# Kernel optimization log

Measured on AMD Instinct MI355X. Metric: run time of the kernel, lower is better.

The kernel has to match this reference:

```python
import jax, jax.numpy as jnp
import numpy as np

DIM = 48
NUM_HEADS = 8
DIM_HEAD = DIM // NUM_HEADS
SCALE = DIM_HEAD ** -0.5
EPS = 1e-12  # torch F.normalize eps
DN = ('NCHW', 'OIHW', 'NCHW')


def setup_inputs() -> dict:
    key = jax.random.key(0)
    k1, k2, k3, k4 = jax.random.split(key, 4)
    x = jax.random.normal(k1, (8, DIM, 256, 256), dtype=jnp.float32)
    w_qkv = jax.random.normal(k2, (3 * DIM, DIM, 1, 1), dtype=jnp.float32) * 0.05
    w_dw = jax.random.normal(k3, (3 * DIM, 1, 3, 3), dtype=jnp.float32) * 0.05
    w_proj = jax.random.normal(k4, (DIM, DIM, 1, 1), dtype=jnp.float32) * 0.05
    return {"x": x, "w_qkv": w_qkv, "w_dw": w_dw, "w_proj": w_proj}


def _l2norm(t):
    # torch F.normalize(dim=-1): t / max(||t||_2, eps)
    n = jnp.sqrt(jnp.sum(t * t, axis=-1, keepdims=True))
    return t / jnp.maximum(n, EPS)


def reference(x, w_qkv, w_dw, w_proj):
    b, c, h, w = x.shape
    # 1x1 pointwise conv -> 3*dim channels
    qkv = jax.lax.conv_general_dilated(x, w_qkv, (1, 1), 'SAME', dimension_numbers=DN)
    # 3x3 depthwise conv (groups = 3*dim)
    qkv = jax.lax.conv_general_dilated(qkv, w_dw, (1, 1), 'SAME',
                                       dimension_numbers=DN,
                                       feature_group_count=3 * c)
    q, k, v = jnp.split(qkv, 3, axis=1)
    # [b, heads, dim_head, h*w]
    q = q.reshape(b, NUM_HEADS, DIM_HEAD, h * w)
    k = k.reshape(b, NUM_HEADS, DIM_HEAD, h * w)
    v = v.reshape(b, NUM_HEADS, DIM_HEAD, h * w)
    q = _l2norm(q)
    k = _l2norm(k)
    # channel-wise transposed attention: [b, heads, dim_head, dim_head]
    attn = jnp.einsum('bhdn,bhen->bhde', q, k) * SCALE
    attn = jax.nn.softmax(attn, axis=-1)
    out = jnp.einsum('bhde,bhen->bhdn', attn, v)
    out = out.reshape(b, c, h, w)
    out = jax.lax.conv_general_dilated(out, w_proj, (1, 1), 'SAME', dimension_numbers=DN)
    return out
```

## Files before the change

### kernel.cpp

```cpp
#include <hip/hip_runtime.h>
#include <hip/hip_fp16.h>
#include <math.h>

#define SCALE 0.4082482904638631f

#define BATCH 8
#define HW    256
#define NPIX  65536

#define QKV_H_SIZE ((size_t)BATCH*144*NPIX)
#define VP_H_SIZE  ((size_t)BATCH*48*NPIX)
#define F_BYTE_OFF ((QKV_H_SIZE + VP_H_SIZE) * 2)
#define GP_SIZE    (BATCH*32*8*48)
#define M_SIZE     (BATCH*48*48)

struct __align__(16) H8 { __half h[8]; };

__global__ void kt_w1t(const float* __restrict__ w1, float* __restrict__ w1t)
{
  for (int i = threadIdx.x; i < 144 * 48; i += 256) {
    const int ic = i / 144, oc = i - ic * 144;
    w1t[i] = w1[oc * 48 + ic];
  }
}

__global__ __launch_bounds__(256, 4) void ka_conv1(
    const float* __restrict__ x, const float* __restrict__ w1t,
    __half* __restrict__ qkv)
{
  const int g = blockIdx.x * 256 + threadIdx.x;
  const int b = g >> 16;
  const int n = g & 65535;
  const float* xb = x + ((size_t)b * 48) * NPIX + n;
  __half* ob = qkv + ((size_t)b * 144) * NPIX + n;

  float xr[48];
#pragma unroll
  for (int ic = 0; ic < 48; ++ic) xr[ic] = xb[(size_t)ic * NPIX];
#pragma unroll
  for (int ic = 0; ic < 48; ++ic) asm volatile("" : "+v"(xr[ic]));

#pragma unroll 1
  for (int chunk = 0; chunk < 6; ++chunk) {
    const int oc0 = chunk * 24;
    float acc[24];
#pragma unroll
    for (int j = 0; j < 24; ++j) acc[j] = 0.0f;
#pragma unroll
    for (int ic = 0; ic < 48; ++ic) {
      const float* wrow = w1t + ic * 144 + oc0;
      const float xv = xr[ic];
#pragma unroll
      for (int j = 0; j < 24; ++j) acc[j] = fmaf(wrow[j], xv, acc[j]);
    }
#pragma unroll
    for (int j = 0; j < 24; ++j)
      ob[(size_t)(oc0 + j) * NPIX] = __float2half(acc[j]);
  }
}

__global__ __launch_bounds__(256, 2) void kb_qk(
    const __half* __restrict__ qkv, const float* __restrict__ wd,
    float* __restrict__ gram_part)
{
  __shared__ __align__(16) unsigned char smem[63360];
  __half* st  = (__half*)smem;
  float*  red = (float*)smem;
  float*  pr  = (float*)(smem + 53248);

  const int blk  = blockIdx.x;
  const int band = blk & 31;
  const int h    = (blk >> 5) & 7;
  const int b    = blk >> 8;
  const int y0   = band * 8;
  const int tid  = threadIdx.x;
  const int g    = tid & 31;
  const int rl   = tid >> 5;
  const int x0   = g * 8;

  const __half* qb = qkv + ((size_t)b * 144) * NPIX;
#pragma unroll
  for (int j = 0; j < 15; ++j) {
    const int cid = tid + j * 256;
    const int ch  = cid / 320;
    const int rem = cid - ch * 320;
    const int r   = rem >> 5;
    const int c16 = rem & 31;
    const int gch = (ch < 6) ? (6 * h + ch) : (42 + 6 * h + ch);
    const int grow = y0 - 1 + r;
    H8 v;
    if ((unsigned)grow < 256u) {
      v = *(const H8*)(qb + (size_t)gch * NPIX + grow * 256 + c16 * 8);
    } else {
#pragma unroll
      for (int q = 0; q < 8; ++q) v.h[q] = __float2half(0.0f);
    }
    *(H8*)(st + (ch * 10 + r) * 264 + c16 * 8) = v;
  }
  __syncthreads();

  auto dwrow = [&](int chslot, int gch, float o[8]) {
    const float* w9 = wd + gch * 9;
#pragma unroll
    for (int p = 0; p < 8; ++p) o[p] = 0.0f;
#pragma unroll
    for (int dr = 0; dr < 3; ++dr) {
      const __half* rowp = st + (chslot * 10 + rl + dr) * 264;
      float wn[10];
      wn[0] = (g > 0) ? __half2float(rowp[x0 - 1]) : 0.0f;
      const H8 m = *(const H8*)(rowp + x0);
#pragma unroll
      for (int q = 0; q < 8; ++q) wn[q + 1] = __half2float(m.h[q]);
      wn[9] = (g < 31) ? __half2float(rowp[x0 + 8]) : 0.0f;
#pragma unroll
      for (int dx = 0; dx < 3; ++dx) {
        const float wt = w9[dr * 3 + dx];
#pragma unroll
        for (int p = 0; p < 8; ++p) o[p] = fmaf(wt, wn[p + dx], o[p]);
      }
    }
  };

  float gram[48];
  float qv[6][8];
#pragma unroll
  for (int d = 0; d < 6; ++d) {
    dwrow(d, 6 * h + d, qv[d]);
    float s = 0.0f;
#pragma unroll
    for (int p = 0; p < 8; ++p) s = fmaf(qv[d][p], qv[d][p], s);
    gram[d] = s;
  }
#pragma unroll
  for (int e = 0; e < 6; ++e) {
    float kv[8];
    dwrow(6 + e, 48 + 6 * h + e, kv);
    float s = 0.0f;
#pragma unroll
    for (int p = 0; p < 8; ++p) s = fmaf(kv[p], kv[p], s);
    gram[6 + e] = s;
#pragma unroll
    for (int d = 0; d < 6; ++d) {
      float t = 0.0f;
#pragma unroll
      for (int p = 0; p < 8; ++p) t = fmaf(qv[d][p], kv[p], t);
      gram[12 + 6 * d + e] = t;
    }
  }
  __syncthreads();

  float4* wrow4 = (float4*)(red + tid * 52);
#pragma unroll
  for (int j = 0; j < 12; ++j)
    wrow4[j] = make_float4(gram[4 * j], gram[4 * j + 1], gram[4 * j + 2], gram[4 * j + 3]);
  __syncthreads();

  if (tid < 192) {
    const int vv = tid >> 2, ch = tid & 3;
    float s = 0.0f;
    const float* base = red + (ch * 64) * 52 + vv;
    for (int p = 0; p < 64; ++p) s += base[p * 52];
    pr[vv * 4 + ch] = s;
  }
  __syncthreads();
  if (tid < 48)
    gram_part[(((size_t)b * 32 + band) * 8 + h) * 48 + tid] =
        pr[tid * 4] + pr[tid * 4 + 1] + pr[tid * 4 + 2] + pr[tid * 4 + 3];
}

__global__ __launch_bounds__(256) void kb_v(
    const __half* __restrict__ qkv, const float* __restrict__ wd,
    __half* __restrict__ vp_ws)
{
  __shared__ __align__(16) __half st[34 * 264];

  const int blk  = blockIdx.x;
  const int band = blk & 7;
  const int ch   = (blk >> 3) % 48;
  const int b    = blk / (48 * 8);
  const int y0   = band * 32;
  const int tid  = threadIdx.x;
  const int g    = tid & 31;
  const int rl   = tid >> 5;
  const int x0   = g * 8;
  const int gch  = 96 + ch;

  const __half* plane = qkv + ((size_t)b * 144 + gch) * NPIX;
#pragma unroll
  for (int j = 0; j < 5; ++j) {
    const int cid = tid + j * 256;
    if (cid < 1088) {
      const int r   = cid >> 5;
      const int c16 = cid & 31;
      const int grow = y0 - 1 + r;
      H8 v;
      if ((unsigned)grow < 256u) {
        v = *(const H8*)(plane + grow * 256 + c16 * 8);
      } else {
#pragma unroll
        for (int q = 0; q < 8; ++q) v.h[q] = __float2half(0.0f);
      }
      *(H8*)(st + r * 264 + c16 * 8) = v;
    }
  }
  __syncthreads();

  const float* w9 = wd + gch * 9;
  __half* outp = vp_ws + ((size_t)b * 48 + ch) * NPIX;
#pragma unroll
  for (int i = 0; i < 4; ++i) {
    const int r_out = rl + 8 * i;
    float o[8];
#pragma unroll
    for (int p = 0; p < 8; ++p) o[p] = 0.0f;
#pragma unroll
    for (int dr = 0; dr < 3; ++dr) {
      const __half* rowp = st + (r_out + dr) * 264;
      float wn[10];
      wn[0] = (g > 0) ? __half2float(rowp[x0 - 1]) : 0.0f;
      const H8 m = *(const H8*)(rowp + x0);
#pragma unroll
      for (int q = 0; q < 8; ++q) wn[q + 1] = __half2float(m.h[q]);
      wn[9] = (g < 31) ? __half2float(rowp[x0 + 8]) : 0.0f;
#pragma unroll
      for (int dx = 0; dx < 3; ++dx) {
        const float wt = w9[dr * 3 + dx];
#pragma unroll
        for (int p = 0; p < 8; ++p) o[p] = fmaf(wt, wn[p + dx], o[p]);
      }
    }
    H8 hv;
#pragma unroll
    for (int p = 0; p < 8; ++p) hv.h[p] = __float2half(o[p]);
    *(H8*)(outp + (y0 + r_out) * 256 + x0) = hv;
  }
}

__global__ void kd_attn(const float* __restrict__ gram_part,
                        const float* __restrict__ wp, float* __restrict__ Mmat)
{
  const int b = blockIdx.x >> 3;
  const int h = blockIdx.x & 7;
  __shared__ float S[48];
  __shared__ float attn[36];
  const int tid = threadIdx.x;

  if (tid < 48) {
    float s = 0.0f;
    for (int t = 0; t < 32; ++t)
      s += gram_part[(((size_t)b * 32 + t) * 8 + h) * 48 + tid];
    S[tid] = s;
  }
  __syncthreads();
  if (tid < 36) {
    const int d = tid / 6, e = tid - 6 * d;
    const float nq = fmaxf(sqrtf(S[d]),     1e-12f);
    const float nk = fmaxf(sqrtf(S[6 + e]), 1e-12f);
    attn[tid] = S[12 + tid] / (nq * nk) * SCALE;
  }
  __syncthreads();
  if (tid < 6) {
    float m = attn[tid * 6];
    for (int e = 1; e < 6; ++e) m = fmaxf(m, attn[tid * 6 + e]);
    float ex[6]; float sum = 0.0f;
    for (int e = 0; e < 6; ++e) { ex[e] = expf(attn[tid * 6 + e] - m); sum += ex[e]; }
    const float inv = 1.0f / sum;
    for (int e = 0; e < 6; ++e) attn[tid * 6 + e] = ex[e] * inv;
  }
  __syncthreads();
  for (int i = tid; i < 288; i += 64) {
    const int c = i / 6, e = i - 6 * (i / 6);
    float s = 0.0f;
#pragma unroll
    for (int d = 0; d < 6; ++d) s += wp[c * 48 + 6 * h + d] * attn[d * 6 + e];
    Mmat[((size_t)b * 48 + c) * 48 + 6 * h + e] = s;
  }
}

__global__ __launch_bounds__(256, 4) void ke_out(
    const __half* __restrict__ vp_ws, const float* __restrict__ Mmat,
    float* __restrict__ y)
{
  const int b = blockIdx.x >> 8;
  const int n = ((blockIdx.x & 255) << 8) + threadIdx.x;
  const __half* vb = vp_ws + ((size_t)b * 48) * NPIX + n;
  const float* Mb = Mmat + (size_t)b * 2304;
  float vv[48];
#pragma unroll
  for (int c = 0; c < 48; ++c) vv[c] = __half2float(vb[(size_t)c * NPIX]);
  float* yb = y + ((size_t)b * 48) * NPIX + n;
#pragma unroll 4
  for (int c = 0; c < 48; ++c) {
    float s = 0.0f;
#pragma unroll
    for (int cc = 0; cc < 48; ++cc) s = fmaf(Mb[c * 48 + cc], vv[cc], s);
    yb[(size_t)c * NPIX] = s;
  }
}

extern "C" void kernel_launch(void* const* d_in, const int* in_sizes, int n_in,
                              void* d_out, int out_size, void* d_ws, size_t ws_size,
                              hipStream_t stream)
{
  const float* x  = (const float*)d_in[0];
  const float* w1 = (const float*)d_in[1];
  const float* wd = (const float*)d_in[2];
  const float* wp = (const float*)d_in[3];

  __half* qkv = (__half*)d_ws;
  __half* vp  = qkv + QKV_H_SIZE;
  float*  fw  = (float*)((char*)d_ws + F_BYTE_OFF);
  float*  gp   = fw;
  float*  Mmat = fw + GP_SIZE;
  float*  w1t  = Mmat + M_SIZE;

  hipLaunchKernelGGL(kt_w1t,   dim3(1),    dim3(256), 0, stream, w1, w1t);
  hipLaunchKernelGGL(ka_conv1, dim3(2048), dim3(256), 0, stream, x, w1t, qkv);
  hipLaunchKernelGGL(kb_qk,    dim3(2048), dim3(256), 0, stream, qkv, wd, gp);
  hipLaunchKernelGGL(kb_v,     dim3(3072), dim3(256), 0, stream, qkv, wd, vp);
  hipLaunchKernelGGL(kd_attn,  dim3(64),   dim3(64),  0, stream, gp, wp, Mmat);
  hipLaunchKernelGGL(ke_out,   dim3(2048), dim3(256), 0, stream, vp, Mmat, (float*)d_out);
}
```

Baseline: 426.1 us.

## Compute pointwise qkv conv with split-fp16 MFMA instead of scalar FMA

Replaces the scalar FP32 1x1 conv kernel with an MFMA 16x16x32 fp16 kernel. Weights and inputs are each split into high and low fp16 parts, and three MFMA products per K-chunk approximate fp32 accuracy. Weight fragments are built in LDS by each block, which removes the separate weight-transpose launch. The costs are extra conversion work, duplicated weight prep in every block, and 2-byte strided output stores that may coalesce poorly.

```diff
diff --git a/kernel.cpp b/kernel.cpp
--- a/kernel.cpp
+++ b/kernel.cpp
@@ -16,46 +16,100 @@
 
 struct __align__(16) H8 { __half h[8]; };
 
-__global__ void kt_w1t(const float* __restrict__ w1, float* __restrict__ w1t)
-{
-  for (int i = threadIdx.x; i < 144 * 48; i += 256) {
-    const int ic = i / 144, oc = i - ic * 144;
-    w1t[i] = w1[oc * 48 + ic];
-  }
-}
-
-__global__ __launch_bounds__(256, 4) void ka_conv1(
-    const float* __restrict__ x, const float* __restrict__ w1t,
+typedef _Float16 f16x8 __attribute__((ext_vector_type(8)));
+typedef float    f32x4 __attribute__((ext_vector_type(4)));
+
+#define MFMA16(A,B,C) __builtin_amdgcn_mfma_f32_16x16x32_f16((A),(B),(C),0,0,0)
+
+__global__ __launch_bounds__(256) void ka_mfma(
+    const float* __restrict__ x, const float* __restrict__ w1,
     __half* __restrict__ qkv)
 {
-  const int g = blockIdx.x * 256 + threadIdx.x;
-  const int b = g >> 16;
-  const int n = g & 65535;
-  const float* xb = x + ((size_t)b * 48) * NPIX + n;
-  __half* ob = qkv + ((size_t)b * 144) * NPIX + n;
-
-  float xr[48];
-#pragma unroll
-  for (int ic = 0; ic < 48; ++ic) xr[ic] = xb[(size_t)ic * NPIX];
-#pragma unroll
-  for (int ic = 0; ic < 48; ++ic) asm volatile("" : "+v"(xr[ic]));
+  __shared__ __align__(16) _Float16 Alds[36 * 64 * 8];
+
+  const int tid = threadIdx.x;
+
+  for (int s = tid; s < 18 * 64; s += 256) {
+    const int f  = s >> 6;
+    const int l  = s & 63;
+    const int m  = f >> 1;
+    const int kf = f & 1;
+    const int oc = m * 16 + (l & 15);
+    const int kb = kf * 32 + (l >> 4) * 8;
+    f16x8 ah, al;
+    if (kf == 0 || (l >> 4) < 2) {
+      const float* wp8 = w1 + oc * 48 + kb;
+#pragma unroll
+      for (int j = 0; j < 8; ++j) {
+        const float wv = wp8[j];
+        const _Float16 h = (_Float16)wv;
+        ah[j] = h;
+        al[j] = (_Float16)(wv - (float)h);
+      }
+    } else {
+#pragma unroll
+      for (int j = 0; j < 8; ++j) { ah[j] = (_Float16)0.0f; al[j] = (_Float16)0.0f; }
+    }
+    *(f16x8*)&Alds[(size_t)s * 8]          = ah;
+    *(f16x8*)&Alds[(size_t)(1152 + s) * 8] = al;
+  }
+  __syncthreads();
+
+  const int wv = tid >> 6;
+  const int l  = tid & 63;
+  const int px0 = blockIdx.x * 512 + wv * 128;
+  const int b   = px0 >> 16;
+  const int n0  = px0 & 65535;
+  const float* xb = x   + ((size_t)b * 48)  * NPIX + n0 + (l & 15);
+  __half*      ob = qkv + ((size_t)b * 144) * NPIX + n0 + (l & 15);
+  const int kr   = (l >> 4) * 8;
+  const bool blo = (l < 32);
 
 #pragma unroll 1
-  for (int chunk = 0; chunk < 6; ++chunk) {
-    const int oc0 = chunk * 24;
-    float acc[24];
-#pragma unroll
-    for (int j = 0; j < 24; ++j) acc[j] = 0.0f;
-#pragma unroll
-    for (int ic = 0; ic < 48; ++ic) {
-      const float* wrow = w1t + ic * 144 + oc0;
-      const float xv = xr[ic];
-#pragma unroll
-      for (int j = 0; j < 24; ++j) acc[j] = fmaf(wrow[j], xv, acc[j]);
-    }
-#pragma unroll
-    for (int j = 0; j < 24; ++j)
-      ob[(size_t)(oc0 + j) * NPIX] = __float2half(acc[j]);
+  for (int t = 0; t < 8; ++t) {
+    const int coff = t * 16;
+
+    float xv0[8], xv1[8];
+#pragma unroll
+    for (int j = 0; j < 8; ++j) xv0[j] = xb[(size_t)(kr + j) * NPIX + coff];
+    if (blo) {
+#pragma unroll
+      for (int j = 0; j < 8; ++j) xv1[j] = xb[(size_t)(32 + kr + j) * NPIX + coff];
+    } else {
+#pragma unroll
+      for (int j = 0; j < 8; ++j) xv1[j] = 0.0f;
+    }
+    f16x8 bh0, bl0, bh1, bl1;
+#pragma unroll
+    for (int j = 0; j < 8; ++j) {
+      const _Float16 h0 = (_Float16)xv0[j];
+      bh0[j] = h0;
+      bl0[j] = (_Float16)(xv0[j] - (float)h0);
+      const _Float16 h1 = (_Float16)xv1[j];
+      bh1[j] = h1;
+      bl1[j] = (_Float16)(xv1[j] - (float)h1);
+    }
+
+#pragma unroll
+    for (int m = 0; m < 9; ++m) {
+      const int s0 = (m * 2 + 0) * 64 + l;
+      const int s1 = (m * 2 + 1) * 64 + l;
+      const f16x8 ah0 = *(const f16x8*)&Alds[(size_t)s0 * 8];
+      const f16x8 al0 = *(const f16x8*)&Alds[(size_t)(1152 + s0) * 8];
+      const f16x8 ah1 = *(const f16x8*)&Alds[(size_t)s1 * 8];
+      const f16x8 al1 = *(const f16x8*)&Alds[(size_t)(1152 + s1) * 8];
+      f32x4 c;
+      c[0] = 0.0f; c[1] = 0.0f; c[2] = 0.0f; c[3] = 0.0f;
+      c = MFMA16(ah0, bh0, c);
+      c = MFMA16(ah0, bl0, c);
+      c = MFMA16(al0, bh0, c);
+      c = MFMA16(ah1, bh1, c);
+      c = MFMA16(ah1, bl1, c);
+      c = MFMA16(al1, bh1, c);
+#pragma unroll
+      for (int r = 0; r < 4; ++r)
+        ob[(size_t)(m * 16 + (l >> 4) * 4 + r) * NPIX + coff] = __float2half(c[r]);
+    }
   }
 }
 
@@ -312,12 +366,10 @@
   float*  fw  = (float*)((char*)d_ws + F_BYTE_OFF);
   float*  gp   = fw;
   float*  Mmat = fw + GP_SIZE;
-  float*  w1t  = Mmat + M_SIZE;
-
-  hipLaunchKernelGGL(kt_w1t,   dim3(1),    dim3(256), 0, stream, w1, w1t);
-  hipLaunchKernelGGL(ka_conv1, dim3(2048), dim3(256), 0, stream, x, w1t, qkv);
-  hipLaunchKernelGGL(kb_qk,    dim3(2048), dim3(256), 0, stream, qkv, wd, gp);
-  hipLaunchKernelGGL(kb_v,     dim3(3072), dim3(256), 0, stream, qkv, wd, vp);
-  hipLaunchKernelGGL(kd_attn,  dim3(64),   dim3(64),  0, stream, gp, wp, Mmat);
-  hipLaunchKernelGGL(ke_out,   dim3(2048), dim3(256), 0, stream, vp, Mmat, (float*)d_out);
-}
+
+  hipLaunchKernelGGL(ka_mfma, dim3(1024), dim3(256), 0, stream, x, w1, qkv);
+  hipLaunchKernelGGL(kb_qk,   dim3(2048), dim3(256), 0, stream, qkv, wd, gp);
+  hipLaunchKernelGGL(kb_v,    dim3(3072), dim3(256), 0, stream, qkv, wd, vp);
+  hipLaunchKernelGGL(kd_attn, dim3(64),   dim3(64),  0, stream, gp, wp, Mmat);
+  hipLaunchKernelGGL(ke_out,  dim3(2048), dim3(256), 0, stream, vp, Mmat, (float*)d_out);
+}
```

New measurement: 433.8 us. No clear change (+1.8%).
